# Performance work log

Hardware: AMD Instinct MI355X
Metric: run time of the kernel (lower is better)

Reference implementation:

```python
import jax, jax.numpy as jnp
from jax import lax
import numpy as np

B, S, IN = 8, 4096, 64
D, H, K = 512, 8, 3
TCN_CH = [256, 256, 512]
HD = D // H


def setup_inputs() -> dict:
    key = jax.random.key(0)
    ks = iter(jax.random.split(key, 64))
    def nrm(shape, s=0.02):
        return jax.random.normal(next(ks), shape, jnp.float32) * s
    inp = {"x": jax.random.normal(next(ks), (B, S, IN), jnp.float32)}
    inp["W_in"] = nrm((IN, D)); inp["b_in"] = jnp.zeros((D,), jnp.float32)
    chans = [D] + TCN_CH
    for i in range(3):
        cin, cout = chans[i], chans[i + 1]
        inp[f"c1w{i}"] = nrm((cout, cin, K), 0.01); inp[f"c1b{i}"] = jnp.zeros((cout,), jnp.float32)
        inp[f"c2w{i}"] = nrm((cout, cout, K), 0.01); inp[f"c2b{i}"] = jnp.zeros((cout,), jnp.float32)
        if cin != cout:  # downsample 1x1 conv (blocks 0 and 2)
            inp[f"dsw{i}"] = nrm((cout, cin, 1), 0.01); inp[f"dsb{i}"] = jnp.zeros((cout,), jnp.float32)
    inp["W_tcn"] = nrm((TCN_CH[-1], D)); inp["b_tcn"] = jnp.zeros((D,), jnp.float32)
    NL = 2  # attention layers, stacked on leading axis
    for n in ["Wq", "Wk", "Wv", "Wo"]:
        inp[n] = nrm((NL, D, D))
    for n in ["bq", "bk", "bv", "bo", "ln_b"]:
        inp[n] = jnp.zeros((NL, D), jnp.float32)
    inp["ln_g"] = jnp.ones((NL, D), jnp.float32)
    inp["W_out"] = nrm((D, 1)); inp["b_out"] = jnp.zeros((1,), jnp.float32)
    return inp


def _conv(x, w, b, dil, pad):
    # x: (B,C,L), w: (O,I,K)
    y = lax.conv_general_dilated(x, w, (1,), [(pad, pad)], rhs_dilation=(dil,),
                                 dimension_numbers=("NCH", "OIH", "NCH"))
    return y + b[None, :, None]


def _block(t, c1w, c1b, c2w, c2b, ds, dil):
    # TemporalConvBlock: symmetric padding (k-1)*dil on both convs, truncate to input length
    pad = (K - 1) * dil
    o = jax.nn.relu(_conv(t, c1w, c1b, dil, pad))   # length L + pad
    o = _conv(o, c2w, c2b, dil, pad)                # length L + 2*pad
    r = t if ds is None else _conv(t, ds[0], ds[1], 1, 0)
    return jax.nn.relu(o[:, :, : t.shape[2]] + r)


def _layernorm(x, g, b, eps=1e-5):
    mu = x.mean(-1, keepdims=True)
    var = ((x - mu) ** 2).mean(-1, keepdims=True)
    return (x - mu) * lax.rsqrt(var + eps) * g + b


def _forward(x, W_in, b_in, c1w0, c1b0, c2w0, c2b0, dsw0, dsb0,
             c1w1, c1b1, c2w1, c2b1, c1w2, c1b2, c2w2, c2b2, dsw2, dsb2,
             W_tcn, b_tcn, Wq, bq, Wk, bk, Wv, bv, Wo, bo, ln_g, ln_b, W_out, b_out):
    h = x @ W_in + b_in                              # (B,S,D)
    t = jnp.swapaxes(h, 1, 2)                        # (B,D,S)
    t = _block(t, c1w0, c1b0, c2w0, c2b0, (dsw0, dsb0), 1)
    t = _block(t, c1w1, c1b1, c2w1, c2b1, None, 2)
    t = _block(t, c1w2, c1b2, c2w2, c2b2, (dsw2, dsb2), 4)
    h = h + jnp.swapaxes(t, 1, 2) @ W_tcn + b_tcn
    # sinusoidal positional encoding
    pos = jnp.arange(S, dtype=jnp.float32)[:, None]
    div = jnp.exp(jnp.arange(0, D, 2, dtype=jnp.float32) * (-np.log(10000.0) / D))
    pe = jnp.stack([jnp.sin(pos * div), jnp.cos(pos * div)], axis=-1).reshape(S, D)
    h = h + pe[None]
    for l in range(Wq.shape[0]):
        res = h
        def heads(y):  # (B,S,D) -> (B,H,S,HD)
            return y.reshape(B, S, H, HD).transpose(0, 2, 1, 3)
        q = heads(h @ Wq[l] + bq[l])
        k = heads(h @ Wk[l] + bk[l])
        v = heads(h @ Wv[l] + bv[l])
        qf = jax.nn.elu(q) + 1.0
        kf = jax.nn.elu(k) + 1.0
        kv = jnp.einsum("bhnd,bhnm->bhdm", kf, v)            # (B,H,HD,HD)
        out = jnp.einsum("bhnd,bhdm->bhnm", qf, kv)          # (B,H,S,HD)
        norm = jnp.maximum(jnp.einsum("bhnd,bhd->bhn", qf, kf.sum(2)), 1e-6)
        out = out / norm[..., None]
        out = out.transpose(0, 2, 1, 3).reshape(B, S, D)
        h = _layernorm(res + out @ Wo[l] + bo[l], ln_g[l], ln_b[l])
    pooled = h.mean(1)                                       # (B,D)
    return (pooled @ W_out + b_out)[:, 0]                    # (B,)


def reference(x, W_in, b_in, c1w0, c1b0, c2w0, c2b0, dsw0, dsb0,
              c1w1, c1b1, c2w1, c2b1, c1w2, c1b2, c2w2, c2b2, dsw2, dsb2,
              W_tcn, b_tcn, Wq, bq, Wk, bk, Wv, bv, Wo, bo, ln_g, ln_b, W_out, b_out):
    return _forward(x, W_in, b_in, c1w0, c1b0, c2w0, c2b0, dsw0, dsb0,
                    c1w1, c1b1, c2w1, c2b1, c1w2, c1b2, c2w2, c2b2, dsw2, dsb2,
                    W_tcn, b_tcn, Wq, bq, Wk, bk, Wv, bv, Wo, bo, ln_g, ln_b, W_out, b_out)
```

## Files before the change

### kernel.cpp

```cpp
#include <hip/hip_runtime.h>

typedef unsigned short u16;
typedef unsigned int u32;
typedef short bhalf8 __attribute__((ext_vector_type(8)));
typedef float f32x4 __attribute__((ext_vector_type(4)));

#define S_LEN 4096
#define NSEG 30

__device__ __forceinline__ float b2f(u16 h){ return __uint_as_float(((u32)h) << 16); }
__device__ __forceinline__ u16 f2b(float f){
  u32 u = __float_as_uint(f);
  return (u16)((u + 0x7FFFu + ((u >> 16) & 1u)) >> 16);
}
__device__ __forceinline__ u32 cvtpk(float a, float b){
  u32 r; asm("v_cvt_pk_bf16_f32 %0, %1, %2" : "=v"(r) : "v"(a), "v"(b)); return r;
}
__device__ __forceinline__ void unp8(uint4 v, float* f){
  f[0]=__uint_as_float(v.x<<16); f[1]=__uint_as_float(v.x&0xffff0000u);
  f[2]=__uint_as_float(v.y<<16); f[3]=__uint_as_float(v.y&0xffff0000u);
  f[4]=__uint_as_float(v.z<<16); f[5]=__uint_as_float(v.z&0xffff0000u);
  f[6]=__uint_as_float(v.w<<16); f[7]=__uint_as_float(v.w&0xffff0000u);
}
__device__ __forceinline__ void unp4(uint2 v, float* f){
  f[0]=__uint_as_float(v.x<<16); f[1]=__uint_as_float(v.x&0xffff0000u);
  f[2]=__uint_as_float(v.y<<16); f[3]=__uint_as_float(v.y&0xffff0000u);
}

__device__ __forceinline__ size_t taddr(int r, int c, int C){
  return (size_t)(r >> 7) * ((size_t)C << 7) + (size_t)((c >> 5) << 12)
       + ((r & 127) << 5) + (c & 31);
}

__device__ __forceinline__ void gload16(const void* g, void* l){
  __builtin_amdgcn_global_load_lds(
      (__attribute__((address_space(1))) void*)(g),
      (__attribute__((address_space(3))) void*)(l), 16, 0, 0);
}

struct PrepArgs {
  const float* src[NSEG];
  int N[NSEG]; int K[NSEG]; int sn[NSEG]; int sk[NSEG]; unsigned off[NSEG];
};

__global__ __launch_bounds__(256) void prep_w(PrepArgs pa, u16* __restrict__ wb){
  int seg = blockIdx.y;
  int N = pa.N[seg], K = pa.K[seg];
  int ntk = (K + 31) >> 5;
  int tiles = ((N + 31) >> 5) * ntk;
  int tile = blockIdx.x;
  if (tile >= tiles) return;
  int n0 = (tile / ntk) << 5, k0 = (tile % ntk) << 5;
  const float* src = pa.src[seg];
  long sn = pa.sn[seg], sk = pa.sk[seg];
  u16* dst = wb + pa.off[seg];
  int lk = threadIdx.x & 31, ln = threadIdx.x >> 5;
  #pragma unroll
  for (int i = 0; i < 4; ++i){
    int n = n0 + ln + i*8, k = k0 + lk;
    if (n < N && k < K)
      dst[(size_t)n*K + k] = f2b(src[(long)n*sn + (long)k*sk]);
  }
}

__global__ __launch_bounds__(256) void pe_k(float* __restrict__ pe){
  int id = blockIdx.x*256 + threadIdx.x;
  int s = id >> 8, i = id & 255;
  float div = expf((float)i * (-2.0f * 9.210340371976184f / 512.0f));
  float a = (float)s * div;
  pe[(size_t)s*512 + 2*i]   = sinf(a);
  pe[(size_t)s*512 + 2*i+1] = cosf(a);
}

__global__ __launch_bounds__(256) void cvt_k(const float* __restrict__ x, u16* __restrict__ xb, int n){
  int id = blockIdx.x*256 + threadIdx.x;
  if (id < n){
    int r = id >> 6, c = id & 63;
    xb[taddr(r, c, 64)] = f2b(x[id]);
  }
}

template<int KTOT>
__global__ __launch_bounds__(512, 1) void gemm8_k(
    const u16* __restrict__ A, const u16* __restrict__ W,
    const float* __restrict__ bias, const float* __restrict__ bias2,
    const float* __restrict__ bias3,
    u16* __restrict__ out, const u16* __restrict__ resb,
    const float* __restrict__ peb,
    int N, int nN, int flags)
{
  constexpr int KT = KTOT >> 6;
  constexpr int IT = KT >> 1;
  __shared__ u16 As[2][16384];
  __shared__ u16 Bs[2][16384];
  const int tid = threadIdx.x;
  const int wave = tid >> 6, lane = tid & 63;
  const int wm = wave >> 2, wn = wave & 3;
  const int c0 = lane >> 4, fro = lane & 15;

  const int nwg = gridDim.x;
  const int lin = blockIdx.x;
  const int swz = (lin & 7) * (nwg >> 3) + (lin >> 3);
  const int mb = swz / nN, nb = swz - mb * nN;
  const int m0 = mb << 8, n0 = nb << 8;

  const f32x4 zf = {0.f,0.f,0.f,0.f};
  f32x4 acc[8][4];
  #pragma unroll
  for (int i=0;i<8;++i)
    #pragma unroll
    for (int j=0;j<4;++j) acc[i][j] = zf;

  bhalf8 af[2][2], bf[4][2];

  auto SA = [&](int t, int q){
    int s = (q << 9) + tid;
    int row = s >> 3, phys = s & 7;
    int lc = phys ^ (row & 7);
    int grow = m0 + row;
    int gcol = (t << 6) + (lc << 3);
    size_t ga = ((size_t)(grow >> 7) << 16) + (size_t)((gcol >> 5) << 12)
              + ((grow & 127) << 5) + (gcol & 31);
    gload16(A + ga, &As[t & 1][(q << 12) + (wave << 9)]);
  };
  auto SB = [&](int t, int j){
    int s = (j << 9) + tid;
    int row = s >> 3, phys = s & 7;
    int lc = phys ^ (row & 7);
    gload16(W + (size_t)(n0 + row) * KTOT + (t << 6) + (lc << 3),
            &Bs[t & 1][(j << 12) + (wave << 9)]);
  };
  auto LDB = [&](int t){
    #pragma unroll
    for (int nt=0;nt<4;++nt)
      #pragma unroll
      for (int ks=0;ks<2;++ks){
        int row = (wn << 6) + (nt << 4) + fro;
        int phys = ((ks << 2) + c0) ^ (row & 7);
        bf[nt][ks] = *(const bhalf8*)&Bs[t & 1][(row << 6) + (phys << 3)];
      }
  };
  auto LDA = [&](int t, int q){
    #pragma unroll
    for (int mtl=0;mtl<2;++mtl)
      #pragma unroll
      for (int ks=0;ks<2;++ks){
        int row = (q << 6) + (wm << 5) + (mtl << 4) + fro;
        int phys = ((ks << 2) + c0) ^ (row & 7);
        af[mtl][ks] = *(const bhalf8*)&As[t & 1][(row << 6) + (phys << 3)];
      }
  };
  auto BAR = [&]{
    __builtin_amdgcn_sched_barrier(0);
    __builtin_amdgcn_s_barrier();
    __builtin_amdgcn_sched_barrier(0);
  };
  auto MM = [&](int q){
    __builtin_amdgcn_s_setprio(1);
    #pragma unroll
    for (int mtl=0;mtl<2;++mtl)
      #pragma unroll
      for (int nt=0;nt<4;++nt){
        acc[(q<<1)+mtl][nt] = __builtin_amdgcn_mfma_f32_16x16x32_bf16(
            bf[nt][0], af[mtl][0], acc[(q<<1)+mtl][nt], 0, 0, 0);
        acc[(q<<1)+mtl][nt] = __builtin_amdgcn_mfma_f32_16x16x32_bf16(
            bf[nt][1], af[mtl][1], acc[(q<<1)+mtl][nt], 0, 0, 0);
      }
    __builtin_amdgcn_s_setprio(0);
  };

  #pragma unroll
  for (int x=0;x<4;++x){ SA(0,x); SB(0,x); }
  #pragma unroll
  for (int x=0;x<3;++x){ SA(1,x); SB(1,x); }
  asm volatile("s_waitcnt vmcnt(6)" ::: "memory");
  BAR();

  #pragma unroll
  for (int i=0;i<IT;++i){
    const int t0 = 2*i, t1 = 2*i+1, t2 = 2*i+2, t3 = 2*i+3;
    #pragma unroll
    for (int q=0;q<4;++q){
      if (q == 0) LDB(t0);
      LDA(t0, q);
      if (q == 0){ SA(t1,3); SB(t1,3); }
      else if (t2 < KT){ SA(t2,q-1); SB(t2,q-1); }
      BAR();
      MM(q);
      if (q == 3){
        if (t2 < KT) asm volatile("s_waitcnt vmcnt(6)" ::: "memory");
        else         asm volatile("s_waitcnt vmcnt(0)" ::: "memory");
      }
      BAR();
    }
    #pragma unroll
    for (int q=0;q<4;++q){
      if (q == 0) LDB(t1);
      LDA(t1, q);
      if (q == 0){ if (t2 < KT){ SA(t2,3); SB(t2,3); } }
      else if (t3 < KT){ SA(t3,q-1); SB(t3,q-1); }
      BAR();
      MM(q);
      if (q == 3 && (i + 1 < IT))
        asm volatile("s_waitcnt vmcnt(6)" ::: "memory");
      BAR();
    }
  }

  const int th = n0 >> 9;
  #pragma unroll
  for (int mt = 0; mt < 8; ++mt){
    const int row = m0 + ((mt >> 1) << 6) + (wm << 5) + ((mt & 1) << 4) + fro;
    const size_t prow = (size_t)(row & (S_LEN - 1)) * 512;
    #pragma unroll
    for (int nt = 0; nt < 4; ++nt){
      const int col = n0 + (wn << 6) + (nt << 4) + (c0 << 2);
      float v0 = acc[mt][nt][0], v1 = acc[mt][nt][1], v2 = acc[mt][nt][2], v3 = acc[mt][nt][3];
      if (flags & 32){
        const float* bp = (th == 0) ? bias : ((th == 1) ? bias2 : bias3);
        if (bp){ float4 b4 = *(const float4*)&bp[col & 511]; v0+=b4.x; v1+=b4.y; v2+=b4.z; v3+=b4.w; }
      } else {
        if (bias){ float4 b4 = *(const float4*)&bias[col]; v0+=b4.x; v1+=b4.y; v2+=b4.z; v3+=b4.w; }
      }
      if (flags & 4){
        uint2 rv = *(const uint2*)(resb + taddr(row, col, N));
        float rf[4]; unp4(rv, rf);
        v0 += rf[0]; v1 += rf[1]; v2 += rf[2]; v3 += rf[3];
      }
      if (flags & 8){
        float4 p4 = *(const float4*)&peb[prow + col];
        v0 += p4.x; v1 += p4.y; v2 += p4.z; v3 += p4.w;
      }
      if (flags & 1){
        v0 = fmaxf(v0, 0.f); v1 = fmaxf(v1, 0.f); v2 = fmaxf(v2, 0.f); v3 = fmaxf(v3, 0.f);
      }
      if ((flags & 2) && (!(flags & 32) || th < 2)){
        v0 = (v0 > 0.f) ? (v0 + 1.f) : __expf(v0);
        v1 = (v1 > 0.f) ? (v1 + 1.f) : __expf(v1);
        v2 = (v2 > 0.f) ? (v2 + 1.f) : __expf(v2);
        v3 = (v3 > 0.f) ? (v3 + 1.f) : __expf(v3);
      }
      uint2 pk; pk.x = cvtpk(v0, v1); pk.y = cvtpk(v2, v3);
      *(uint2*)(out + taddr(row, col, N)) = pk;
    }
  }
}

template<int NTAPS, int KS1, int KS2>
__global__ __launch_bounds__(256) void gemm_k(
    const u16* __restrict__ A, const u16* __restrict__ W,
    const u16* __restrict__ A2, const u16* __restrict__ W2,
    const float* __restrict__ bias, const float* __restrict__ bias2,
    const float* __restrict__ bias3,
    u16* __restrict__ out, const u16* __restrict__ resb,
    const float* __restrict__ peb, const float* __restrict__ den,
    int N, int CA, int CA2, int dil, int nN, int wbstride, int flags)
{
  constexpr bool MT   = (NTAPS == 3);
  constexpr int HALO  = MT ? 8 : 0;
  constexpr int AR    = MT ? 144 : 128;
  constexpr int DA    = MT ? ((KS2 > 0) ? 3 : 2) : 3;
  constexpr int DB    = 3;
  constexpr int K     = KS1 << 5;
  constexpr int K2    = KS2 << 5;
  constexpr int TOTAL = MT ? (3*KS1 + KS2) : (KS1 + KS2);
  __shared__ u16 As[DA][AR*32];
  __shared__ u16 Bs[DB][128*32];
  const int tid = threadIdx.x;
  const int wave = tid >> 6, lane = tid & 63;
  const int wm = wave >> 1, wn = wave & 1;

  const int nwg = gridDim.x;
  const int lin = blockIdx.x;
  const int swz = (lin & 7) * (nwg >> 3) + (lin >> 3);
  const int mb = swz / nN, nb = swz - mb * nN;
  const int m0 = mb << 7, n0 = nb << 7;
  const bool bnd = (m0 & (S_LEN - 1)) == 0;

  const u16* Ae = (flags & 16) ? (A + (((size_t)(n0 & 511) >> 5) << 12)) : A;

  const int lr4 = lane >> 2, lc4 = lane & 3;
  const int c0 = lane >> 4, fro = lane & 15;

  const f32x4 zf = {0.f, 0.f, 0.f, 0.f};
  const bhalf8 zb = {0,0,0,0,0,0,0,0};
  f32x4 acc[4][4];
  #pragma unroll
  for (int i=0;i<4;++i)
    #pragma unroll
    for (int j=0;j<4;++j) acc[i][j] = zf;

  const u16* Wb = W + (size_t)(m0 >> 12) * (size_t)wbstride;
  const size_t abase  = (size_t)mb * ((size_t)CA  << 7);
  const size_t abase2 = (size_t)mb * ((size_t)CA2 << 7);

  auto STAGE_A = [&](int kb, int ab){
    const size_t tb = abase + ((size_t)kb << 12);
    #pragma unroll
    for (int half = 0; half < 2; ++half){
      int mrow = (wave << 5) + (half << 4) + lr4;
      int i = mrow + HALO;
      int cg = lc4 ^ ((i >> 1) & 3);
      gload16(Ae + tb + mrow*32 + (cg << 3), &As[ab][(HALO + (wave << 5) + (half << 4)) * 32]);
    }
    if (MT && wave == 0 && lane < 32){
      int j = lr4;
      int cg = lc4 ^ ((j >> 1) & 3);
      size_t hb_ = (mb ? abase - ((size_t)CA << 7) : abase) + ((size_t)kb << 12) + (120 + j)*32;
      gload16(Ae + hb_ + (cg << 3), &As[ab][0]);
    }
  };
  auto STAGE_A2 = [&](int t2, int ab){
    const size_t tb = abase2 + ((size_t)t2 << 12);
    #pragma unroll
    for (int half = 0; half < 2; ++half){
      int mrow = (wave << 5) + (half << 4) + lr4;
      int i = mrow + HALO;
      int cg = lc4 ^ ((i >> 1) & 3);
      gload16(A2 + tb + mrow*32 + (cg << 3), &As[ab][(HALO + (wave << 5) + (half << 4)) * 32]);
    }
  };
  auto STAGE_B = [&](const u16* Wt, size_t kstride, int kb, int bb){
    #pragma unroll
    for (int half = 0; half < 2; ++half){
      int i = (wave << 5) + (half << 4) + lr4;
      int cg = lc4 ^ ((i >> 1) & 3);
      gload16(Wt + (size_t)(n0 + i) * kstride + (kb << 5) + (cg << 3),
              &Bs[bb][((wave << 5) + (half << 4)) * 32]);
    }
  };
  auto DO16 = [&](int ab, int bb, int sh, bool mask){
    bhalf8 af[4], bf[4];
    #pragma unroll
    for (int mt = 0; mt < 4; ++mt){
      int r8 = (wm << 6) + (mt << 4) + fro + HALO + sh;
      af[mt] = *(const bhalf8*)&As[ab][r8 * 32 + ((c0 ^ ((r8 >> 1) & 3)) << 3)];
    }
    if (MT && mask && bnd && wm == 0 && fro + sh < 0) af[0] = zb;
    #pragma unroll
    for (int nt = 0; nt < 4; ++nt){
      int rB = (wn << 6) + (nt << 4) + fro;
      bf[nt] = *(const bhalf8*)&Bs[bb][rB * 32 + ((c0 ^ ((rB >> 1) & 3)) << 3)];
    }
    #pragma unroll
    for (int mt = 0; mt < 4; ++mt)
      #pragma unroll
      for (int nt = 0; nt < 4; ++nt)
        acc[mt][nt] = __builtin_amdgcn_mfma_f32_16x16x32_bf16(bf[nt], af[mt], acc[mt][nt], 0, 0, 0);
  };

  if constexpr (!MT){
    auto STG = [&](int s){
      int b = s % 3;
      if (s < KS1){ STAGE_A(s, b); STAGE_B(Wb, (size_t)K, s, b); }
      else if (KS2 > 0){ STAGE_A2(s - KS1, b); STAGE_B(W2, (size_t)K2, s - KS1, b); }
    };
    STG(0);
    if constexpr (TOTAL > 1) STG(1);
    #pragma unroll
    for (int s = 0; s < TOTAL; ++s){
      if (s + 1 >= TOTAL) asm volatile("s_waitcnt vmcnt(0)" ::: "memory");
      else                asm volatile("s_waitcnt vmcnt(4)" ::: "memory");
      __builtin_amdgcn_sched_barrier(0);
      __builtin_amdgcn_s_barrier();
      __builtin_amdgcn_sched_barrier(0);
      if (s + 2 < TOTAL) STG(s + 2);
      DO16(s % 3, s % 3, 0, false);
    }
  } else {
    auto STG = [&](int s){
      if (s < 3*KS1){
        int kb = s / 3, tap = s % 3;
        if (tap == 0) STAGE_A(kb, kb % DA);
        STAGE_B(Wb + (size_t)tap * N * K, (size_t)K, kb, s % 3);
      } else if (KS2 > 0){
        int t2 = s - 3*KS1;
        STAGE_A2(t2, (KS1 + t2) % DA);
        STAGE_B(W2, (size_t)K2, t2, s % 3);
      }
    };
    STG(0);
    if constexpr (TOTAL > 1) STG(1);
    #pragma unroll
    for (int s = 0; s < TOTAL; ++s){
      if (s + 1 >= TOTAL) asm volatile("s_waitcnt vmcnt(0)" ::: "memory");
      else                asm volatile("s_waitcnt vmcnt(2)" ::: "memory");
      __builtin_amdgcn_sched_barrier(0);
      __builtin_amdgcn_s_barrier();
      __builtin_amdgcn_sched_barrier(0);
      if (s + 2 < TOTAL) STG(s + 2);
      if (s < 3*KS1) DO16((s/3) % DA, s % 3, ((s%3) - 2) * dil, true);
      else           DO16((KS1 + (s - 3*KS1)) % DA, s % 3, 0, false);
    }
  }

  const int mb_l = (wm << 6) + fro;
  const int cb_l = (wn << 6) + (c0 << 2);
  const int th = n0 >> 9;
  #pragma unroll
  for (int mt = 0; mt < 4; ++mt){
    const int row = m0 + mb_l + (mt << 4);
    const size_t prow = (size_t)(row & (S_LEN - 1)) * 512;
    #pragma unroll
    for (int nt = 0; nt < 4; ++nt){
      const int col = n0 + cb_l + (nt << 4);
      float v0 = acc[mt][nt][0], v1 = acc[mt][nt][1], v2 = acc[mt][nt][2], v3 = acc[mt][nt][3];
      if (flags & 32){
        const float* bp = (th == 0) ? bias : ((th == 1) ? bias2 : bias3);
        if (bp){ float4 b4 = *(const float4*)&bp[col & 511]; v0+=b4.x; v1+=b4.y; v2+=b4.z; v3+=b4.w; }
      } else {
        if (bias) { float4 b4 = *(const float4*)&bias[col];  v0+=b4.x; v1+=b4.y; v2+=b4.z; v3+=b4.w; }
        if (bias2){ float4 b4 = *(const float4*)&bias2[col]; v0+=b4.x; v1+=b4.y; v2+=b4.z; v3+=b4.w; }
      }
      if (flags & 4){
        uint2 rv = *(const uint2*)(resb + taddr(row, col, N));
        float rf[4]; unp4(rv, rf);
        v0 += rf[0]; v1 += rf[1]; v2 += rf[2]; v3 += rf[3];
      }
      if (flags & 8){
        float4 p4 = *(const float4*)&peb[prow + col];
        v0 += p4.x; v1 += p4.y; v2 += p4.z; v3 += p4.w;
      }
      if (flags & 16){
        float d = fmaxf(den[((size_t)row << 3) + (col >> 6)], 1e-6f);
        float rd = 1.0f / d;
        v0 *= rd; v1 *= rd; v2 *= rd; v3 *= rd;
      }
      if (flags & 1){
        v0 = fmaxf(v0, 0.f); v1 = fmaxf(v1, 0.f); v2 = fmaxf(v2, 0.f); v3 = fmaxf(v3, 0.f);
      }
      if ((flags & 2) && (!(flags & 32) || th < 2)){
        v0 = (v0 > 0.f) ? (v0 + 1.f) : __expf(v0);
        v1 = (v1 > 0.f) ? (v1 + 1.f) : __expf(v1);
        v2 = (v2 > 0.f) ? (v2 + 1.f) : __expf(v2);
        v3 = (v3 > 0.f) ? (v3 + 1.f) : __expf(v3);
      }
      uint2 pk; pk.x = cvtpk(v0, v1); pk.y = cvtpk(v2, v3);
      *(uint2*)(out + taddr(row, col, N)) = pk;
    }
  }
}

__global__ __launch_bounds__(256) void kv_partial(
    const u16* __restrict__ qkv,
    float* __restrict__ kvp, float* __restrict__ ksp)
{
  const int bh = blockIdx.x;
  const int b = bh >> 3, h = bh & 7;
  const int ch = blockIdx.y;
  const int t = threadIdx.x;
  __shared__ u16 kfs[2][16][64];
  __shared__ u16 vs[2][16][64];
  float acc[4][4] = {{0.f}};
  float ks[4] = {0.f,0.f,0.f,0.f};
  const int d0 = (t >> 4) << 2;
  const int c0 = (t & 15) << 2;
  const int lr = t >> 4, lc = (t & 15) << 2;
  const int rowbase = (b << 12) + (ch << 9);
  const int ck = 512 + (h << 6) + lc;
  const int cv = 1024 + (h << 6) + lc;

  uint2 rk = *(const uint2*)(qkv + taddr(rowbase + lr, ck, 1536));
  uint2 rv = *(const uint2*)(qkv + taddr(rowbase + lr, cv, 1536));
  *(uint2*)&kfs[0][lr][lc] = rk;
  *(uint2*)&vs[0][lr][lc]  = rv;
  __syncthreads();
  int cur = 0;
  for (int g = 0; g < 32; ++g){
    if (g + 1 < 32){
      int r = rowbase + ((g + 1) << 4) + lr;
      rk = *(const uint2*)(qkv + taddr(r, ck, 1536));
      rv = *(const uint2*)(qkv + taddr(r, cv, 1536));
    }
    #pragma unroll
    for (int i = 0; i < 16; ++i){
      float kv4[4], vv4[4];
      unp4(*(const uint2*)&kfs[cur][i][d0], kv4);
      unp4(*(const uint2*)&vs[cur][i][c0], vv4);
      #pragma unroll
      for (int j=0;j<4;++j)
        #pragma unroll
        for (int k2=0;k2<4;++k2) acc[j][k2] += kv4[j]*vv4[k2];
      if ((t & 15) == 0){
        #pragma unroll
        for (int j=0;j<4;++j) ks[j] += kv4[j];
      }
    }
    if (g + 1 < 32){
      *(uint2*)&kfs[cur ^ 1][lr][lc] = rk;
      *(uint2*)&vs[cur ^ 1][lr][lc]  = rv;
    }
    __syncthreads();
    cur ^= 1;
  }
  float* dst = kvp + ((size_t)(bh << 3) + ch) * 4096;
  #pragma unroll
  for (int j=0;j<4;++j)
    #pragma unroll
    for (int k2=0;k2<4;++k2) dst[(d0+j)*64 + (c0+k2)] = acc[j][k2];
  if ((t & 15) == 0){
    float* kd = ksp + ((size_t)(bh << 3) + ch) * 64;
    #pragma unroll
    for (int j=0;j<4;++j) kd[d0+j] = ks[j];
  }
}

__global__ __launch_bounds__(256) void kvred_k(
    const float* __restrict__ kvp, const float* __restrict__ ksp,
    float* __restrict__ kvf, float* __restrict__ ksf)
{
  int bh = blockIdx.x, t = threadIdx.x;
  for (int e = t; e < 4096; e += 256){
    float s = 0.f;
    #pragma unroll
    for (int ch = 0; ch < 8; ++ch) s += kvp[((size_t)(bh<<3)+ch)*4096 + e];
    kvf[(size_t)bh*4096 + e] = s;
  }
  if (t < 64){
    float s = 0.f;
    #pragma unroll
    for (int ch = 0; ch < 8; ++ch) s += ksp[((size_t)(bh<<3)+ch)*64 + t];
    ksf[bh*64 + t] = s;
  }
}

__global__ __launch_bounds__(256) void denpack_k(const u16* __restrict__ qkv,
    const float* __restrict__ ksf, float* __restrict__ den,
    const float* __restrict__ kvf, u16* __restrict__ wbd)
{
  int bid = blockIdx.x;
  if (bid < 1024){
    int id = bid*256 + threadIdx.x;
    int r = id >> 3, h = id & 7;
    int b = r >> 12;
    const float* ks = ksf + ((b<<3)+h)*64;
    float s = 0.f;
    for (int d = 0; d < 64; d += 8){
      uint4 vq = *(const uint4*)(qkv + taddr(r, (h << 6) + d, 1536));
      float f[8]; unp8(vq, f);
      #pragma unroll
      for (int j=0;j<8;++j) s += f[j]*ks[d+j];
    }
    den[id] = s;
  } else {
    int id = (bid - 1024)*256 + threadIdx.x;
    int b = id >> 16;
    int n = (id >> 7) & 511, j = id & 127;
    float v = 0.f;
    if ((j >> 6) == ((n >> 6) & 1))
      v = kvf[((size_t)((b<<3)+(n>>6)))*4096 + (j & 63)*64 + (n & 63)];
    wbd[id] = f2b(v);
  }
}

__global__ __launch_bounds__(256) void ln_k(const u16* __restrict__ in,
    const float* __restrict__ g, const float* __restrict__ beta, u16* __restrict__ out)
{
  int wave = threadIdx.x >> 6, lane = threadIdx.x & 63;
  int row = blockIdx.x*4 + wave;
  size_t ad = taddr(row, lane*8, 512);
  uint4 pv = *(const uint4*)(in + ad);
  float f[8]; unp8(pv, f);
  float s = 0.f, ss = 0.f;
  #pragma unroll
  for (int i=0;i<8;++i){ s += f[i]; ss += f[i]*f[i]; }
  for (int m=1;m<64;m<<=1){ s += __shfl_xor(s,m); ss += __shfl_xor(ss,m); }
  float mean = s * (1.f/512.f);
  float var = ss * (1.f/512.f) - mean*mean;
  float rstd = rsqrtf(fmaxf(var, 0.f) + 1e-5f);
  u16 o[8];
  #pragma unroll
  for (int i=0;i<8;++i){
    int c = lane*8 + i;
    o[i] = f2b((f[i]-mean)*rstd*g[c] + beta[c]);
  }
  *(uint4*)(out + ad) = *(uint4*)o;
}

__global__ __launch_bounds__(256) void pool1_k(const u16* __restrict__ hb,
    const float* __restrict__ wout, const float* __restrict__ g,
    const float* __restrict__ beta, float* __restrict__ part)
{
  int b = blockIdx.x >> 6, ch = blockIdx.x & 63;
  int t = threadIdx.x;
  __shared__ float ws[512];
  __shared__ float red[256];
  __shared__ float S2[2];
  float a0 = 0.f, a1 = 0.f;
  for (int i = t; i < 512; i += 256){
    float w = wout[i];
    float gw = w * g[i];
    ws[i] = gw;
    a0 += gw;
    a1 += w * beta[i];
  }
  red[t] = a0; __syncthreads();
  for (int k2=128;k2;k2>>=1){ if (t<k2) red[t]+=red[t+k2]; __syncthreads(); }
  if (!t) S2[0] = red[0];
  __syncthreads();
  red[t] = a1; __syncthreads();
  for (int k2=128;k2;k2>>=1){ if (t<k2) red[t]+=red[t+k2]; __syncthreads(); }
  if (!t) S2[1] = red[0];
  __syncthreads();
  const float Sgw = S2[0], Sbw = S2[1];

  int r = (b << 12) + (ch << 6) + (t >> 2);
  int c0 = (t & 3) << 7;
  float sd = 0.f, s1 = 0.f, s2 = 0.f;
  for (int i = 0; i < 128; i += 8){
    uint4 v = *(const uint4*)(hb + taddr(r, c0 + i, 512));
    float f[8]; unp8(v, f);
    #pragma unroll
    for (int j=0;j<8;++j){ float x = f[j]; sd += x*ws[c0+i+j]; s1 += x; s2 += x*x; }
  }
  sd += __shfl_xor(sd,1); s1 += __shfl_xor(s1,1); s2 += __shfl_xor(s2,1);
  sd += __shfl_xor(sd,2); s1 += __shfl_xor(s1,2); s2 += __shfl_xor(s2,2);
  float mean = s1 * (1.f/512.f);
  float var  = s2 * (1.f/512.f) - mean*mean;
  float rstd = rsqrtf(fmaxf(var, 0.f) + 1e-5f);
  float rowv = rstd * (sd - mean * Sgw) + Sbw;
  red[t] = ((t & 3) == 0) ? rowv : 0.f;
  __syncthreads();
  for (int k2=128;k2;k2>>=1){ if (t<k2) red[t]+=red[t+k2]; __syncthreads(); }
  if (!t) part[blockIdx.x] = red[0];
}

__global__ __launch_bounds__(64) void pool2_k(const float* __restrict__ part,
    const float* __restrict__ bout, float* __restrict__ out)
{
  int b = blockIdx.x, t = threadIdx.x;
  float s = part[(b << 6) + t];
  for (int m=1;m<64;m<<=1) s += __shfl_xor(s,m);
  if (!t) out[b] = s * (1.f/4096.f) + bout[0];
}

extern "C" void kernel_launch(void* const* d_in, const int* in_sizes, int n_in,
                              void* d_out, int out_size, void* d_ws, size_t ws_size,
                              hipStream_t stream)
{
  (void)in_sizes; (void)n_in; (void)out_size; (void)ws_size;
  const float* x    = (const float*)d_in[0];
  const float* W_in = (const float*)d_in[1];
  const float* b_in = (const float*)d_in[2];
  const float* c1w0 = (const float*)d_in[3];
  const float* c1b0 = (const float*)d_in[4];
  const float* c2w0 = (const float*)d_in[5];
  const float* c2b0 = (const float*)d_in[6];
  const float* dsw0 = (const float*)d_in[7];
  const float* dsb0 = (const float*)d_in[8];
  const float* c1w1 = (const float*)d_in[9];
  const float* c1b1 = (const float*)d_in[10];
  const float* c2w1 = (const float*)d_in[11];
  const float* c2b1 = (const float*)d_in[12];
  const float* c1w2 = (const float*)d_in[13];
  const float* c1b2 = (const float*)d_in[14];
  const float* c2w2 = (const float*)d_in[15];
  const float* c2b2 = (const float*)d_in[16];
  const float* dsw2 = (const float*)d_in[17];
  const float* dsb2 = (const float*)d_in[18];
  const float* W_tcn= (const float*)d_in[19];
  const float* b_tcn= (const float*)d_in[20];
  const float* Wq   = (const float*)d_in[21];
  const float* Wk   = (const float*)d_in[22];
  const float* Wv   = (const float*)d_in[23];
  const float* Wo   = (const float*)d_in[24];
  const float* bq   = (const float*)d_in[25];
  const float* bk   = (const float*)d_in[26];
  const float* bv   = (const float*)d_in[27];
  const float* bo   = (const float*)d_in[28];
  const float* lnb  = (const float*)d_in[29];
  const float* lng  = (const float*)d_in[30];
  const float* W_out= (const float*)d_in[31];
  const float* b_out= (const float*)d_in[32];

  char* base = (char*)d_ws;
  size_t off = 0;
  auto alloc = [&](size_t bytes) -> void* {
    void* p = base + off;
    off += (bytes + 255) & ~(size_t)255;
    return p;
  };
  u16* WB   = (u16*)alloc(4816896ull*2);
  u16* wbd  = (u16*)alloc(8ull*512*128*2);
  float* peb= (float*)alloc(4096ull*512*4);
  float* den= (float*)alloc(32768ull*8*4);
  float* kvp= (float*)alloc(512ull*4096*4);
  float* ksp= (float*)alloc(512ull*64*4);
  float* kvf= (float*)alloc(64ull*4096*4);
  float* ksf= (float*)alloc(64ull*64*4);
  float* part=(float*)alloc(512*4);
  u16* hb   = (u16*)alloc(32768ull*512*2);
  char* qkvR= (char*)alloc(32768ull*1536*2);
  u16* atto = (u16*)alloc(32768ull*512*2);

  u16* qkvb = (u16*)qkvR;
  u16* xb   = (u16*)(qkvR);
  u16* t1b  = (u16*)(qkvR + 4194304);
  u16* t2b  = (u16*)(qkvR + 20971520);
  u16* t3b  = (u16*)(qkvR + 37748736);
  u16* o1b  = atto;

  unsigned wo_ = 0;
  auto wseg = [&](unsigned e){ unsigned o = wo_; wo_ += e; return o; };
  unsigned oWin  = wseg(512*64);
  unsigned oC1w0 = wseg(3*256*512);
  unsigned oC2w0 = wseg(3*256*256);
  unsigned oDs0  = wseg(256*512);
  unsigned oC1w1 = wseg(3*256*256);
  unsigned oC2w1 = wseg(3*256*256);
  unsigned oC1w2 = wseg(3*512*256);
  unsigned oC2w2 = wseg(3*512*512);
  unsigned oDs2  = wseg(512*256);
  unsigned oWtcn = wseg(512*512);
  unsigned oQKV  = wseg(2*1536*512);
  unsigned oWo   = wseg(2*512*512);

  PrepArgs pa;
  int si = 0;
  auto seg = [&](const float* s, int N, int K, int sn, int sk, unsigned o){
    pa.src[si]=s; pa.N[si]=N; pa.K[si]=K; pa.sn[si]=sn; pa.sk[si]=sk; pa.off[si]=o; ++si;
  };
  seg(W_in, 512, 64, 1, 512, oWin);
  for (int t=0;t<3;++t) seg(c1w0 + t, 256, 512, 1536, 3, oC1w0 + t*131072);
  for (int t=0;t<3;++t) seg(c2w0 + t, 256, 256,  768, 3, oC2w0 + t*65536);
  seg(dsw0, 256, 512, 512, 1, oDs0);
  for (int t=0;t<3;++t) seg(c1w1 + t, 256, 256,  768, 3, oC1w1 + t*65536);
  for (int t=0;t<3;++t) seg(c2w1 + t, 256, 256,  768, 3, oC2w1 + t*65536);
  for (int t=0;t<3;++t) seg(c1w2 + t, 512, 256,  768, 3, oC1w2 + t*131072);
  for (int t=0;t<3;++t) seg(c2w2 + t, 512, 512, 1536, 3, oC2w2 + t*262144);
  seg(dsw2, 512, 256, 256, 1, oDs2);
  seg(W_tcn, 512, 512, 1, 512, oWtcn);
  for (int l=0;l<2;++l){
    seg(Wq + l*262144, 512, 512, 1, 512, oQKV + l*786432 + 0);
    seg(Wk + l*262144, 512, 512, 1, 512, oQKV + l*786432 + 262144);
    seg(Wv + l*262144, 512, 512, 1, 512, oQKV + l*786432 + 524288);
  }
  for (int l=0;l<2;++l) seg(Wo + l*262144, 512, 512, 1, 512, oWo + l*262144);

  prep_w<<<dim3(256, NSEG), 256, 0, stream>>>(pa, WB);
  pe_k<<<4096, 256, 0, stream>>>(peb);
  cvt_k<<<8192, 256, 0, stream>>>(x, xb, 32768*64);

  const int RELU=1, ELU1=2, RES=4, PE=8, DIV=16, QKV=32;
  auto gemm = [&](const u16* A, const u16* W, const u16* A2, const u16* W2,
                  const float* b1, const float* b2, const float* b3,
                  u16* out, const u16* resb,
                  int K, int K2, int N, int CA, int CA2, int ntaps,
                  int dil, int wbs, int flags){
    int nN = N >> 7;
    dim3 grid(256 * nN);
    if (ntaps == 3){
      if (K == 512 && K2 == 0)
        gemm_k<3,16,0><<<grid, 256, 0, stream>>>(A, W, A2, W2, b1, b2, b3, out, resb,
                                                 peb, den, N, CA, CA2, dil, nN, wbs, flags);
      else if (K == 256 && K2 == 512)
        gemm_k<3,8,16><<<grid, 256, 0, stream>>>(A, W, A2, W2, b1, b2, b3, out, resb,
                                                 peb, den, N, CA, CA2, dil, nN, wbs, flags);
      else if (K == 256 && K2 == 0)
        gemm_k<3,8,0><<<grid, 256, 0, stream>>>(A, W, A2, W2, b1, b2, b3, out, resb,
                                                peb, den, N, CA, CA2, dil, nN, wbs, flags);
      else
        gemm_k<3,16,8><<<grid, 256, 0, stream>>>(A, W, A2, W2, b1, b2, b3, out, resb,
                                                 peb, den, N, CA, CA2, dil, nN, wbs, flags);
    } else {
      if (K == 64)
        gemm_k<1,2,0><<<grid, 256, 0, stream>>>(A, W, A2, W2, b1, b2, b3, out, resb,
                                                peb, den, N, CA, CA2, dil, nN, wbs, flags);
      else
        gemm_k<1,4,0><<<grid, 256, 0, stream>>>(A, W, A2, W2, b1, b2, b3, out, resb,
                                                peb, den, N, CA, CA2, dil, nN, wbs, flags);
    }
  };
  auto gemm8 = [&](const u16* A, const u16* W, const float* b1, const float* b2,
                   const float* b3, u16* out, const u16* resb, int N, int flags){
    int nN = N >> 8;
    gemm8_k<512><<<dim3(128 * nN), 512, 0, stream>>>(A, W, b1, b2, b3, out, resb,
                                                     peb, N, nN, flags);
  };

  gemm(xb, WB + oWin, nullptr, nullptr, b_in, nullptr, nullptr, hb, nullptr,
       64, 0, 512, 64, 0, 1, 1, 0, 0);
  gemm(hb,  WB + oC1w0, nullptr, nullptr, c1b0, nullptr, nullptr, o1b, nullptr,
       512, 0, 256, 512, 0, 3, 1, 0, RELU);
  gemm(o1b, WB + oC2w0, hb, WB + oDs0, c2b0, dsb0, nullptr, t1b, nullptr,
       256, 512, 256, 256, 512, 3, 1, 0, RELU);
  gemm(t1b, WB + oC1w1, nullptr, nullptr, c1b1, nullptr, nullptr, o1b, nullptr,
       256, 0, 256, 256, 0, 3, 2, 0, RELU);
  gemm(o1b, WB + oC2w1, nullptr, nullptr, c2b1, nullptr, nullptr, t2b, t1b,
       256, 0, 256, 256, 0, 3, 2, 0, RELU|RES);
  gemm(t2b, WB + oC1w2, nullptr, nullptr, c1b2, nullptr, nullptr, o1b, nullptr,
       256, 0, 512, 256, 0, 3, 4, 0, RELU);
  gemm(o1b, WB + oC2w2, t2b, WB + oDs2, c2b2, dsb2, nullptr, t3b, nullptr,
       512, 256, 512, 512, 256, 3, 4, 0, RELU);
  gemm8(t3b, WB + oWtcn, b_tcn, nullptr, nullptr, hb, hb, 512, RES|PE);

  for (int l = 0; l < 2; ++l){
    gemm8(hb, WB + oQKV + l*786432, bq + l*512, bk + l*512, bv + l*512,
          qkvb, nullptr, 1536, ELU1|QKV);
    kv_partial<<<dim3(64, 8), 256, 0, stream>>>(qkvb, kvp, ksp);
    kvred_k<<<64, 256, 0, stream>>>(kvp, ksp, kvf, ksf);
    denpack_k<<<3072, 256, 0, stream>>>(qkvb, ksf, den, kvf, wbd);
    gemm(qkvb, wbd, nullptr, nullptr, nullptr, nullptr, nullptr, atto, nullptr,
         128, 0, 512, 1536, 0, 1, 1, 512*128, DIV);
    gemm8(atto, WB + oWo + l*262144, bo + l*512, nullptr, nullptr, hb, hb, 512, RES);
    if (l == 0)
      ln_k<<<8192, 256, 0, stream>>>(hb, lng, lnb, hb);
  }

  pool1_k<<<512, 256, 0, stream>>>(hb, W_out, lng + 512, lnb + 512, part);
  pool2_k<<<8, 64, 0, stream>>>(part, b_out, (float*)d_out);
}
```

Before: 749.4 us.

## Replace 256x256 gemm8 with 256x128 triple-buffered gemm9 for higher occupancy

Replaces the 256x256-tile, 64-deep-K, double-buffered GEMM used for the TCN projection, QKV and output projections with a 256x128-tile, 32-deep-K kernel that keeps three shared-memory stages and issues one barrier per K step. Launch bounds move from 1 to 4 blocks per SM, and the per-wave accumulator footprint is halved, so more workgroups can be resident and the grid doubles. The cost is lower arithmetic intensity per tile, more global loads of A, and dropping the fine-grained interleaved quarter-step schedule and setprio hints.

```diff
diff --git a/kernel.cpp b/kernel.cpp
--- a/kernel.cpp
+++ b/kernel.cpp
@@ -81,7 +81,7 @@
 }
 
 template<int KTOT>
-__global__ __launch_bounds__(512, 1) void gemm8_k(
+__global__ __launch_bounds__(512, 4) void gemm9_k(
     const u16* __restrict__ A, const u16* __restrict__ W,
     const float* __restrict__ bias, const float* __restrict__ bias2,
     const float* __restrict__ bias3,
@@ -89,128 +89,82 @@
     const float* __restrict__ peb,
     int N, int nN, int flags)
 {
-  constexpr int KT = KTOT >> 6;
-  constexpr int IT = KT >> 1;
-  __shared__ u16 As[2][16384];
-  __shared__ u16 Bs[2][16384];
+  constexpr int KT = KTOT >> 5;
+  __shared__ u16 As[3][8192];
+  __shared__ u16 Bs[3][4096];
   const int tid = threadIdx.x;
   const int wave = tid >> 6, lane = tid & 63;
-  const int wm = wave >> 2, wn = wave & 3;
+  const int wm = wave >> 1, wn = wave & 1;
   const int c0 = lane >> 4, fro = lane & 15;
+  const int sr = tid >> 2, sp = tid & 3;
 
   const int nwg = gridDim.x;
   const int lin = blockIdx.x;
   const int swz = (lin & 7) * (nwg >> 3) + (lin >> 3);
   const int mb = swz / nN, nb = swz - mb * nN;
-  const int m0 = mb << 8, n0 = nb << 8;
+  const int m0 = mb << 8, n0 = nb << 7;
 
   const f32x4 zf = {0.f,0.f,0.f,0.f};
-  f32x4 acc[8][4];
-  #pragma unroll
-  for (int i=0;i<8;++i)
+  f32x4 acc[4][4];
+  #pragma unroll
+  for (int i=0;i<4;++i)
     #pragma unroll
     for (int j=0;j<4;++j) acc[i][j] = zf;
 
-  bhalf8 af[2][2], bf[4][2];
-
-  auto SA = [&](int t, int q){
-    int s = (q << 9) + tid;
-    int row = s >> 3, phys = s & 7;
-    int lc = phys ^ (row & 7);
+  auto SA = [&](int t, int half){
+    int row = (half << 7) + sr;
+    int lc = sp ^ ((row >> 1) & 3);
     int grow = m0 + row;
-    int gcol = (t << 6) + (lc << 3);
-    size_t ga = ((size_t)(grow >> 7) << 16) + (size_t)((gcol >> 5) << 12)
-              + ((grow & 127) << 5) + (gcol & 31);
-    gload16(A + ga, &As[t & 1][(q << 12) + (wave << 9)]);
-  };
-  auto SB = [&](int t, int j){
-    int s = (j << 9) + tid;
-    int row = s >> 3, phys = s & 7;
-    int lc = phys ^ (row & 7);
-    gload16(W + (size_t)(n0 + row) * KTOT + (t << 6) + (lc << 3),
-            &Bs[t & 1][(j << 12) + (wave << 9)]);
-  };
-  auto LDB = [&](int t){
-    #pragma unroll
-    for (int nt=0;nt<4;++nt)
+    size_t ga = ((size_t)(grow >> 7) << 16) + ((size_t)t << 12)
+              + ((grow & 127) << 5) + (lc << 3);
+    gload16(A + ga, &As[t % 3][(half << 12) + (wave << 9)]);
+  };
+  auto SB = [&](int t){
+    int lc = sp ^ ((sr >> 1) & 3);
+    gload16(W + (size_t)(n0 + sr) * KTOT + (t << 5) + (lc << 3),
+            &Bs[t % 3][wave << 9]);
+  };
+  auto STG = [&](int s){ SA(s, 0); SA(s, 1); SB(s); };
+
+  auto CMP = [&](int s){
+    int b = s % 3;
+    bhalf8 af[4], bf[4];
+    #pragma unroll
+    for (int mt = 0; mt < 4; ++mt){
+      int row = (wm << 6) + (mt << 4) + fro;
+      int phys = c0 ^ ((row >> 1) & 3);
+      af[mt] = *(const bhalf8*)&As[b][row * 32 + (phys << 3)];
+    }
+    #pragma unroll
+    for (int nt = 0; nt < 4; ++nt){
+      int row = (wn << 6) + (nt << 4) + fro;
+      int phys = c0 ^ ((row >> 1) & 3);
+      bf[nt] = *(const bhalf8*)&Bs[b][row * 32 + (phys << 3)];
+    }
+    #pragma unroll
+    for (int mt = 0; mt < 4; ++mt)
       #pragma unroll
-      for (int ks=0;ks<2;++ks){
-        int row = (wn << 6) + (nt << 4) + fro;
-        int phys = ((ks << 2) + c0) ^ (row & 7);
-        bf[nt][ks] = *(const bhalf8*)&Bs[t & 1][(row << 6) + (phys << 3)];
-      }
-  };
-  auto LDA = [&](int t, int q){
-    #pragma unroll
-    for (int mtl=0;mtl<2;++mtl)
-      #pragma unroll
-      for (int ks=0;ks<2;++ks){
-        int row = (q << 6) + (wm << 5) + (mtl << 4) + fro;
-        int phys = ((ks << 2) + c0) ^ (row & 7);
-        af[mtl][ks] = *(const bhalf8*)&As[t & 1][(row << 6) + (phys << 3)];
-      }
-  };
-  auto BAR = [&]{
+      for (int nt = 0; nt < 4; ++nt)
+        acc[mt][nt] = __builtin_amdgcn_mfma_f32_16x16x32_bf16(bf[nt], af[mt], acc[mt][nt], 0, 0, 0);
+  };
+
+  STG(0);
+  if (KT > 1) STG(1);
+  #pragma unroll
+  for (int s = 0; s < KT; ++s){
+    if (s + 1 >= KT) asm volatile("s_waitcnt vmcnt(0)" ::: "memory");
+    else             asm volatile("s_waitcnt vmcnt(3)" ::: "memory");
     __builtin_amdgcn_sched_barrier(0);
     __builtin_amdgcn_s_barrier();
     __builtin_amdgcn_sched_barrier(0);
-  };
-  auto MM = [&](int q){
-    __builtin_amdgcn_s_setprio(1);
-    #pragma unroll
-    for (int mtl=0;mtl<2;++mtl)
-      #pragma unroll
-      for (int nt=0;nt<4;++nt){
-        acc[(q<<1)+mtl][nt] = __builtin_amdgcn_mfma_f32_16x16x32_bf16(
-            bf[nt][0], af[mtl][0], acc[(q<<1)+mtl][nt], 0, 0, 0);
-        acc[(q<<1)+mtl][nt] = __builtin_amdgcn_mfma_f32_16x16x32_bf16(
-            bf[nt][1], af[mtl][1], acc[(q<<1)+mtl][nt], 0, 0, 0);
-      }
-    __builtin_amdgcn_s_setprio(0);
-  };
-
-  #pragma unroll
-  for (int x=0;x<4;++x){ SA(0,x); SB(0,x); }
-  #pragma unroll
-  for (int x=0;x<3;++x){ SA(1,x); SB(1,x); }
-  asm volatile("s_waitcnt vmcnt(6)" ::: "memory");
-  BAR();
-
-  #pragma unroll
-  for (int i=0;i<IT;++i){
-    const int t0 = 2*i, t1 = 2*i+1, t2 = 2*i+2, t3 = 2*i+3;
-    #pragma unroll
-    for (int q=0;q<4;++q){
-      if (q == 0) LDB(t0);
-      LDA(t0, q);
-      if (q == 0){ SA(t1,3); SB(t1,3); }
-      else if (t2 < KT){ SA(t2,q-1); SB(t2,q-1); }
-      BAR();
-      MM(q);
-      if (q == 3){
-        if (t2 < KT) asm volatile("s_waitcnt vmcnt(6)" ::: "memory");
-        else         asm volatile("s_waitcnt vmcnt(0)" ::: "memory");
-      }
-      BAR();
-    }
-    #pragma unroll
-    for (int q=0;q<4;++q){
-      if (q == 0) LDB(t1);
-      LDA(t1, q);
-      if (q == 0){ if (t2 < KT){ SA(t2,3); SB(t2,3); } }
-      else if (t3 < KT){ SA(t3,q-1); SB(t3,q-1); }
-      BAR();
-      MM(q);
-      if (q == 3 && (i + 1 < IT))
-        asm volatile("s_waitcnt vmcnt(6)" ::: "memory");
-      BAR();
-    }
+    if (s + 2 < KT) STG(s + 2);
+    CMP(s);
   }
 
   const int th = n0 >> 9;
   #pragma unroll
-  for (int mt = 0; mt < 8; ++mt){
-    const int row = m0 + ((mt >> 1) << 6) + (wm << 5) + ((mt & 1) << 4) + fro;
+  for (int mt = 0; mt < 4; ++mt){
+    const int row = m0 + (wm << 6) + (mt << 4) + fro;
     const size_t prow = (size_t)(row & (S_LEN - 1)) * 512;
     #pragma unroll
     for (int nt = 0; nt < 4; ++nt){
@@ -771,10 +725,10 @@
                                                 peb, den, N, CA, CA2, dil, nN, wbs, flags);
     }
   };
-  auto gemm8 = [&](const u16* A, const u16* W, const float* b1, const float* b2,
+  auto gemm9 = [&](const u16* A, const u16* W, const float* b1, const float* b2,
                    const float* b3, u16* out, const u16* resb, int N, int flags){
-    int nN = N >> 8;
-    gemm8_k<512><<<dim3(128 * nN), 512, 0, stream>>>(A, W, b1, b2, b3, out, resb,
+    int nN = N >> 7;
+    gemm9_k<512><<<dim3(128 * nN), 512, 0, stream>>>(A, W, b1, b2, b3, out, resb,
                                                      peb, N, nN, flags);
   };
 
@@ -792,17 +746,17 @@
        256, 0, 512, 256, 0, 3, 4, 0, RELU);
   gemm(o1b, WB + oC2w2, t2b, WB + oDs2, c2b2, dsb2, nullptr, t3b, nullptr,
        512, 256, 512, 512, 256, 3, 4, 0, RELU);
-  gemm8(t3b, WB + oWtcn, b_tcn, nullptr, nullptr, hb, hb, 512, RES|PE);
+  gemm9(t3b, WB + oWtcn, b_tcn, nullptr, nullptr, hb, hb, 512, RES|PE);
 
   for (int l = 0; l < 2; ++l){
-    gemm8(hb, WB + oQKV + l*786432, bq + l*512, bk + l*512, bv + l*512,
+    gemm9(hb, WB + oQKV + l*786432, bq + l*512, bk + l*512, bv + l*512,
           qkvb, nullptr, 1536, ELU1|QKV);
     kv_partial<<<dim3(64, 8), 256, 0, stream>>>(qkvb, kvp, ksp);
     kvred_k<<<64, 256, 0, stream>>>(kvp, ksp, kvf, ksf);
     denpack_k<<<3072, 256, 0, stream>>>(qkvb, ksf, den, kvf, wbd);
     gemm(qkvb, wbd, nullptr, nullptr, nullptr, nullptr, nullptr, atto, nullptr,
          128, 0, 512, 1536, 0, 1, 1, 512*128, DIV);
-    gemm8(atto, WB + oWo + l*262144, bo + l*512, nullptr, nullptr, hb, hb, 512, RES);
+    gemm9(atto, WB + oWo + l*262144, bo + l*512, nullptr, nullptr, hb, hb, 512, RES);
     if (l == 0)
       ln_k<<<8192, 256, 0, stream>>>(hb, lng, lnb, hb);
   }
```

Result: faster. 701.7 us (-6.4%).
